# Optimization experiments

Measured on AMD Instinct MI355X. Metric: run time of the kernel, lower is better.

## Reference

```python
import jax, jax.numpy as jnp
import numpy as np

D = 1024
H = 16
DH = D // H  # 64

def setup_inputs() -> dict:
    key = jax.random.key(0)
    ks = jax.random.split(key, 9)
    B, L = 2, 2048
    s = 1.0 / np.sqrt(D)
    inp = {
        'x':  jax.random.normal(ks[0], (B, L, D), dtype=jnp.float32),
        'Wq': jax.random.uniform(ks[1], (D, D), jnp.float32, -s, s),
        'bq': jnp.zeros((D,), jnp.float32),
        'Wk': jax.random.uniform(ks[2], (D, D), jnp.float32, -s, s),
        'bk': jnp.zeros((D,), jnp.float32),
        'Wv': jax.random.uniform(ks[3], (D, D), jnp.float32, -s, s),
        'bv': jnp.zeros((D,), jnp.float32),
        'Wo': jax.random.uniform(ks[4], (D, D), jnp.float32, -s, s),
        'bo': jnp.zeros((D,), jnp.float32),
    }
    return inp

def reference(x, Wq, bq, Wk, bk, Wv, bv, Wo, bo):
    B, L, _ = x.shape
    # projections (torch Linear: x @ W.T + b; here weights stored as [D_in, D_out])
    q = (x @ Wq + bq).reshape(B, L, H, DH).transpose(0, 2, 1, 3)  # [B,H,L,DH]
    k = (x @ Wk + bk).reshape(B, L, H, DH).transpose(0, 2, 1, 3)
    v = (x @ Wv + bv).reshape(B, L, H, DH).transpose(0, 2, 1, 3)
    scores = jnp.einsum('bhqd,bhkd->bhqk', q, k) / jnp.sqrt(jnp.float32(DH))
    attn = jax.nn.softmax(scores, axis=-1)  # dropout p=0 / eval -> identity
    out = jnp.einsum('bhqk,bhkd->bhqd', attn, v)
    out = out.transpose(0, 2, 1, 3).reshape(B, L, D)
    return out @ Wo + bo
```

## Files before the change

### kernel.cpp

```cpp
#include <hip/hip_runtime.h>
#include <stdint.h>

typedef __attribute__((ext_vector_type(8)))  __bf16 bf16x8;
typedef __attribute__((ext_vector_type(4)))  __bf16 bf16x4;
typedef __attribute__((ext_vector_type(4)))  float  f32x4;
typedef __attribute__((ext_vector_type(16))) float  f32x16;
typedef __attribute__((ext_vector_type(4)))  int    i32x4;

#define DEV static __device__ __forceinline__

DEV float fast_exp2(float x) {
#if __has_builtin(__builtin_amdgcn_exp2f)
  return __builtin_amdgcn_exp2f(x);
#else
  return exp2f(x);
#endif
}

DEV uint32_t pack_bf2(float a, float b) {
  __bf16 x = (__bf16)a, y = (__bf16)b;
  uint16_t xu = __builtin_bit_cast(uint16_t, x);
  uint16_t yu = __builtin_bit_cast(uint16_t, y);
  return (uint32_t)xu | ((uint32_t)yu << 16);
}

DEV void gload_lds16(const void* g, void* l) {
  __builtin_amdgcn_global_load_lds(
      (const __attribute__((address_space(1))) void*)(uintptr_t)(g),
      (__attribute__((address_space(3))) void*)(uint32_t)(uintptr_t)(l),
      16, 0, 0);
}

__global__ void k_cvt_x(const float* __restrict__ x, __bf16* __restrict__ xb, int n) {
  int i = (blockIdx.x * 256 + threadIdx.x) * 4;
  if (i < n) {
    f32x4 v = *(const f32x4*)(x + i);
    bf16x4 o;
    o[0] = (__bf16)v[0]; o[1] = (__bf16)v[1];
    o[2] = (__bf16)v[2]; o[3] = (__bf16)v[3];
    *(bf16x4*)(xb + i) = o;
  }
}

__global__ void k_cvt_wt(const float* __restrict__ W, __bf16* __restrict__ Wt,
                         int K, int N) {
  __shared__ __bf16 T[64][66];
  int t = threadIdx.x;
  int r = t >> 2;
  int cq = (t & 3) << 4;
  {
    int gk = blockIdx.y * 64 + r;
    int gn0 = blockIdx.x * 64 + cq;
    const float* src = W + (size_t)gk * N + gn0;
#pragma unroll
    for (int j = 0; j < 16; j += 4) {
      f32x4 v = *(const f32x4*)(src + j);
#pragma unroll
      for (int jj = 0; jj < 4; ++jj) T[r][cq + j + jj] = (__bf16)v[jj];
    }
  }
  __syncthreads();
  {
    int gn = blockIdx.x * 64 + r;
    int gk0 = blockIdx.y * 64 + cq;
    __bf16* dst = Wt + (size_t)gn * K + gk0;
    bf16x8 o0, o1;
#pragma unroll
    for (int j = 0; j < 8; ++j) { o0[j] = T[cq + j][r]; o1[j] = T[cq + 8 + j][r]; }
    *(bf16x8*)dst = o0;
    *(bf16x8*)(dst + 8) = o1;
  }
}

__global__ void k_vt(const __bf16* __restrict__ qkv, __bf16* __restrict__ Vt) {
  __shared__ __bf16 T[64][66];
  int lt = blockIdx.x, bh = blockIdx.y;
  int b = bh >> 4, h = bh & 15;
  int t = threadIdx.x;
  int r = t >> 2, cq = (t & 3) << 4;
  {
    const __bf16* src = qkv + (size_t)(b * 2048 + lt * 64 + r) * 3072 + 2048 + h * 64 + cq;
    bf16x8 v0 = *(const bf16x8*)src;
    bf16x8 v1 = *(const bf16x8*)(src + 8);
#pragma unroll
    for (int j = 0; j < 8; ++j) { T[r][cq + j] = v0[j]; T[r][cq + 8 + j] = v1[j]; }
  }
  __syncthreads();
  {
    __bf16* dst = Vt + (size_t)(bh * 64 + r) * 2048 + lt * 64 + cq;
    bf16x8 o0, o1;
#pragma unroll
    for (int j = 0; j < 8; ++j) { o0[j] = T[cq + j][r]; o1[j] = T[cq + 8 + j][r]; }
    *(bf16x8*)dst = o0;
    *(bf16x8*)(dst + 8) = o1;
  }
}

template <int OUTMODE>
__global__ void k_gemm(const __bf16* __restrict__ A, const __bf16* __restrict__ Bt,
                       void* __restrict__ Cout, int M, int N, int K,
                       const float* __restrict__ b0, const float* __restrict__ b1,
                       const float* __restrict__ b2) {
  __shared__ __align__(16) __bf16 As[128 * 64];
  __shared__ __align__(16) __bf16 Bs[128 * 64];
  const int t = threadIdx.x, wid = t >> 6, lane = t & 63;
  const int bm = blockIdx.y, bn = blockIdx.x;
  const int wm = wid >> 1, wn = wid & 1;
  const int l15 = lane & 15, l4 = lane >> 4;
  const int rr = lane >> 3, cc = lane & 7;
  f32x4 acc[4][4] = {};
  const int nk = K >> 6;
  for (int kt = 0; kt < nk; ++kt) {
    __syncthreads();
#pragma unroll
    for (int j = 0; j < 4; ++j) {
      int row = wid * 32 + j * 8 + rr;
      int csrc = (cc ^ (row & 7)) * 8;
      gload_lds16(A + (size_t)(bm * 128 + row) * K + kt * 64 + csrc,
                  (char*)As + (wid * 32 + j * 8) * 128);
      gload_lds16(Bt + (size_t)(bn * 128 + row) * K + kt * 64 + csrc,
                  (char*)Bs + (wid * 32 + j * 8) * 128);
    }
    __syncthreads();
#pragma unroll
    for (int kk = 0; kk < 2; ++kk) {
      bf16x8 a[4], b[4];
#pragma unroll
      for (int ms = 0; ms < 4; ++ms) {
        int row = wm * 64 + ms * 16 + l15;
        a[ms] = *(const bf16x8*)((char*)As + row * 128 + (((kk * 4 + l4) ^ (row & 7)) * 16));
      }
#pragma unroll
      for (int ns = 0; ns < 4; ++ns) {
        int row = wn * 64 + ns * 16 + l15;
        b[ns] = *(const bf16x8*)((char*)Bs + row * 128 + (((kk * 4 + l4) ^ (row & 7)) * 16));
      }
#pragma unroll
      for (int ms = 0; ms < 4; ++ms)
#pragma unroll
        for (int ns = 0; ns < 4; ++ns)
          acc[ms][ns] = __builtin_amdgcn_mfma_f32_16x16x32_bf16(a[ms], b[ns], acc[ms][ns], 0, 0, 0);
    }
  }
#pragma unroll
  for (int ms = 0; ms < 4; ++ms) {
#pragma unroll
    for (int ns = 0; ns < 4; ++ns) {
      int n = bn * 128 + wn * 64 + ns * 16 + l15;
      float bias;
      if (OUTMODE == 0) {
        const float* bp = (n < 1024) ? b0 : ((n < 2048) ? b1 : b2);
        bias = bp[n & 1023];
      } else {
        bias = b0[n];
      }
#pragma unroll
      for (int i = 0; i < 4; ++i) {
        int m = bm * 128 + wm * 64 + ms * 16 + l4 * 4 + i;
        float v = acc[ms][ns][i] + bias;
        if (OUTMODE == 0) ((__bf16*)Cout)[(size_t)m * N + n] = (__bf16)v;
        else              ((float*)Cout)[(size_t)m * N + n] = v;
      }
    }
  }
}

__global__ void __launch_bounds__(512, 2)
k_attn(const __bf16* __restrict__ qkv, const __bf16* __restrict__ Vt,
       __bf16* __restrict__ Aout) {
  __shared__ __align__(16) char smem[65536];
  const int t = threadIdx.x, w = t >> 6, lane = t & 63;
  const int wq = w & 3, half = w >> 2;
  const int l31 = lane & 31, hi = lane >> 5;
  const int rr = lane >> 3, cc = lane & 7;
  const int qt = blockIdx.x, bh = blockIdx.y;
  const int b = bh >> 4, h = bh & 15;
  const int kv0 = half * 1024;

  const __bf16* Kg = qkv + (size_t)(b * 2048) * 3072 + 1024 + h * 64;
  const __bf16* Vg = Vt + (size_t)(bh * 64) * 2048;

  bf16x8 aq[4];
  {
    int qrow = b * 2048 + qt * 128 + wq * 32 + l31;
    const __bf16* qp = qkv + (size_t)qrow * 3072 + h * 64 + hi * 8;
#pragma unroll
    for (int d = 0; d < 4; ++d) aq[d] = *(const bf16x8*)(qp + d * 16);
  }

  f32x16 o[2] = {};
  float ls[16];
#pragma unroll
  for (int r = 0; r < 16; ++r) ls[r] = 0.f;
  const float C = 0.18033688f;

  auto STAGE = [&](int bi, int kt) {
    char* Kl = smem + half * 32768 + bi * 16384;
    char* Vl = Kl + 8192;
    const __bf16* kg = Kg + (size_t)(kv0 + kt * 64) * 3072;
    const __bf16* vg = Vg + kv0 + kt * 64;
#pragma unroll
    for (int jj = 0; jj < 2; ++jj) {
      int row = wq * 16 + jj * 8 + rr;
      int csrc = (cc ^ (row & 7)) * 8;
      gload_lds16(kg + (size_t)row * 3072 + csrc, Kl + (wq * 16 + jj * 8) * 128);
      gload_lds16(vg + (size_t)row * 2048 + csrc, Vl + (wq * 16 + jj * 8) * 128);
    }
  };

  STAGE(0, 0);
  __syncthreads();

  int cur = 0;
  for (int kt = 0; kt < 16; ++kt) {
    if (kt < 15) STAGE(cur ^ 1, kt + 1);
    char* Kl = smem + half * 32768 + cur * 16384;
    char* Vl = Kl + 8192;

    f32x16 s[2];
    s[0] = 0.f; s[1] = 0.f;
#pragma unroll
    for (int ks = 0; ks < 2; ++ks) {
      int krow = ks * 32 + l31;
#pragma unroll
      for (int d = 0; d < 4; ++d) {
        bf16x8 kf = *(const bf16x8*)(Kl + krow * 128 + (((d * 2 + hi) ^ (krow & 7)) * 16));
        s[ks] = __builtin_amdgcn_mfma_f32_32x32x16_bf16(kf, aq[d], s[ks], 0, 0, 0);
      }
    }

#pragma unroll
    for (int ks = 0; ks < 2; ++ks)
#pragma unroll
      for (int r = 0; r < 16; ++r)
        s[ks][r] = fast_exp2(s[ks][r] * C);

#pragma unroll
    for (int r = 0; r < 16; ++r) ls[r] += s[0][r] + s[1][r];

    uint32_t W[2][8];
#pragma unroll
    for (int ks = 0; ks < 2; ++ks)
#pragma unroll
      for (int c = 0; c < 8; ++c)
        W[ks][c] = pack_bf2(s[ks][2 * c], s[ks][2 * c + 1]);

#pragma unroll
    for (int kstep = 0; kstep < 4; ++kstep) {
      const int ks = kstep >> 1, base = 4 * (kstep & 1);
      uint32_t w0 = W[ks][base + 0], w1 = W[ks][base + 1];
      uint32_t w2 = W[ks][base + 2], w3 = W[ks][base + 3];
      uint32_t x0 = __shfl_xor((int)w0, 32);
      uint32_t x1 = __shfl_xor((int)w1, 32);
      uint32_t x2 = __shfl_xor((int)w2, 32);
      uint32_t x3 = __shfl_xor((int)w3, 32);
      i32x4 pw;
      pw[0] = (int)(hi ? x2 : w0);
      pw[1] = (int)(hi ? x3 : w1);
      pw[2] = (int)(hi ? w2 : x0);
      pw[3] = (int)(hi ? w3 : x1);
      bf16x8 pa = __builtin_bit_cast(bf16x8, pw);
#pragma unroll
      for (int db = 0; db < 2; ++db) {
        int vrow = db * 32 + l31;
        bf16x8 vf = *(const bf16x8*)(Vl + vrow * 128 + (((kstep * 2 + hi) ^ (vrow & 7)) * 16));
        o[db] = __builtin_amdgcn_mfma_f32_32x32x16_bf16(pa, vf, o[db], 0, 0, 0);
      }
    }

    __syncthreads();
    cur ^= 1;
  }

#pragma unroll
  for (int st = 8; st > 0; st >>= 1)
#pragma unroll
    for (int r = 0; r < st; ++r) ls[r] += ls[r + st];
  float rowsum = ls[0] + __shfl_xor(ls[0], 32);

  float* oLDS = (float*)smem;
  float* sLDS = (float*)(smem + 32768);
  sLDS[w * 64 + lane] = rowsum;
  if (w >= 4) {
    float* ob = oLDS + (w - 4) * 2048;
#pragma unroll
    for (int db = 0; db < 2; ++db)
#pragma unroll
      for (int r = 0; r < 16; ++r)
        ob[(db * 16 + r) * 64 + lane] = o[db][r];
  }
  __syncthreads();
  if (w < 4) {
#pragma unroll
    for (int r = 0; r < 16; ++r) {
      int rowq = (r & 3) + 8 * (r >> 2) + 4 * hi;
      float rs1 = __shfl(rowsum, rowq);
      float rs2 = sLDS[(w + 4) * 64 + rowq];
      float inv = 1.0f / (rs1 + rs2);
      int qg = b * 2048 + qt * 128 + wq * 32 + rowq;
#pragma unroll
      for (int db = 0; db < 2; ++db) {
        float o2 = oLDS[w * 2048 + (db * 16 + r) * 64 + lane];
        float v = (o[db][r] + o2) * inv;
        int col = h * 64 + db * 32 + l31;
        Aout[(size_t)qg * 1024 + col] = (__bf16)v;
      }
    }
  }
}

extern "C" void kernel_launch(void* const* d_in, const int* in_sizes, int n_in,
                              void* d_out, int out_size, void* d_ws, size_t ws_size,
                              hipStream_t stream) {
  const float* x  = (const float*)d_in[0];
  const float* Wq = (const float*)d_in[1];
  const float* bq = (const float*)d_in[2];
  const float* Wk = (const float*)d_in[3];
  const float* bk = (const float*)d_in[4];
  const float* Wv = (const float*)d_in[5];
  const float* bv = (const float*)d_in[6];
  const float* Wo = (const float*)d_in[7];
  const float* bo = (const float*)d_in[8];
  float* out = (float*)d_out;

  char* ws = (char*)d_ws;
  __bf16* xb   = (__bf16*)(ws);
  __bf16* wtq  = (__bf16*)(ws + (8ull  << 20));
  __bf16* wot  = (__bf16*)(ws + (14ull << 20));
  __bf16* qkv  = (__bf16*)(ws + (16ull << 20));
  __bf16* vt   = (__bf16*)(ws + (40ull << 20));
  __bf16* aout = (__bf16*)(ws + (48ull << 20));

  k_cvt_x<<<4096, 256, 0, stream>>>(x, xb, 4096 * 1024);

  dim3 wgrid(16, 16);
  k_cvt_wt<<<wgrid, 256, 0, stream>>>(Wq, wtq,               1024, 1024);
  k_cvt_wt<<<wgrid, 256, 0, stream>>>(Wk, wtq + 1024 * 1024, 1024, 1024);
  k_cvt_wt<<<wgrid, 256, 0, stream>>>(Wv, wtq + 2048 * 1024, 1024, 1024);
  k_cvt_wt<<<wgrid, 256, 0, stream>>>(Wo, wot,               1024, 1024);

  k_gemm<0><<<dim3(24, 32), 256, 0, stream>>>(xb, wtq, qkv, 4096, 3072, 1024, bq, bk, bv);

  k_vt<<<dim3(32, 32), 256, 0, stream>>>(qkv, vt);

  k_attn<<<dim3(16, 32), 512, 0, stream>>>(qkv, vt, aout);

  k_gemm<1><<<dim3(8, 32), 256, 0, stream>>>(aout, wot, out, 4096, 1024, 1024, bo, nullptr, nullptr);
}
```

Measured before the change: 132.5 us.

## Fuse prep kernels, remap attention blocks, reorder K/V LDS layout, add MFMA priority

Merges the x-conversion and four weight-transpose kernels into a single k_prep launch that uses a 3D grid, cutting five launches down to one. The attention grid becomes 1D with a remapped block index so that consecutive blocks share query tiles across 8 heads, which may change L2 locality. The K/V staging now stores tiles in LDS in an MFMA-fragment order instead of the XOR-swizzled row layout, so each lane's fragment read is a contiguous lane*16 offset. It also wraps the MFMA sections in s_setprio to favour matrix issue. The new LDS layout has to match the operand layout exactly, which is a correctness risk.

```diff
diff --git a/kernel.cpp b/kernel.cpp
--- a/kernel.cpp
+++ b/kernel.cpp
@@ -31,44 +31,50 @@
       16, 0, 0);
 }
 
-__global__ void k_cvt_x(const float* __restrict__ x, __bf16* __restrict__ xb, int n) {
-  int i = (blockIdx.x * 256 + threadIdx.x) * 4;
-  if (i < n) {
-    f32x4 v = *(const f32x4*)(x + i);
-    bf16x4 o;
-    o[0] = (__bf16)v[0]; o[1] = (__bf16)v[1];
-    o[2] = (__bf16)v[2]; o[3] = (__bf16)v[3];
-    *(bf16x4*)(xb + i) = o;
-  }
-}
-
-__global__ void k_cvt_wt(const float* __restrict__ W, __bf16* __restrict__ Wt,
-                         int K, int N) {
-  __shared__ __bf16 T[64][66];
-  int t = threadIdx.x;
-  int r = t >> 2;
-  int cq = (t & 3) << 4;
-  {
-    int gk = blockIdx.y * 64 + r;
-    int gn0 = blockIdx.x * 64 + cq;
-    const float* src = W + (size_t)gk * N + gn0;
-#pragma unroll
-    for (int j = 0; j < 16; j += 4) {
-      f32x4 v = *(const f32x4*)(src + j);
-#pragma unroll
-      for (int jj = 0; jj < 4; ++jj) T[r][cq + j + jj] = (__bf16)v[jj];
-    }
-  }
-  __syncthreads();
-  {
-    int gn = blockIdx.x * 64 + r;
-    int gk0 = blockIdx.y * 64 + cq;
-    __bf16* dst = Wt + (size_t)gn * K + gk0;
-    bf16x8 o0, o1;
-#pragma unroll
-    for (int j = 0; j < 8; ++j) { o0[j] = T[cq + j][r]; o1[j] = T[cq + 8 + j][r]; }
-    *(bf16x8*)dst = o0;
-    *(bf16x8*)(dst + 8) = o1;
+__global__ void k_prep(const float* __restrict__ x,  __bf16* __restrict__ xb,
+                       const float* __restrict__ Wq, const float* __restrict__ Wk,
+                       const float* __restrict__ Wv, const float* __restrict__ Wo,
+                       __bf16* __restrict__ wtq, __bf16* __restrict__ wot) {
+  const int z = blockIdx.z;
+  if (z < 4) {
+    const float* W  = (z == 0) ? Wq : (z == 1) ? Wk : (z == 2) ? Wv : Wo;
+    __bf16*      Wt = (z == 3) ? wot : (wtq + (size_t)z * 1024 * 1024);
+    __shared__ __bf16 T[64][66];
+    int t = threadIdx.x;
+    int r = t >> 2;
+    int cq = (t & 3) << 4;
+    {
+      int gk = blockIdx.y * 64 + r;
+      int gn0 = blockIdx.x * 64 + cq;
+      const float* src = W + (size_t)gk * 1024 + gn0;
+#pragma unroll
+      for (int j = 0; j < 16; j += 4) {
+        f32x4 v = *(const f32x4*)(src + j);
+#pragma unroll
+        for (int jj = 0; jj < 4; ++jj) T[r][cq + j + jj] = (__bf16)v[jj];
+      }
+    }
+    __syncthreads();
+    {
+      int gn = blockIdx.x * 64 + r;
+      int gk0 = blockIdx.y * 64 + cq;
+      __bf16* dst = Wt + (size_t)gn * 1024 + gk0;
+      bf16x8 o0, o1;
+#pragma unroll
+      for (int j = 0; j < 8; ++j) { o0[j] = T[cq + j][r]; o1[j] = T[cq + 8 + j][r]; }
+      *(bf16x8*)dst = o0;
+      *(bf16x8*)(dst + 8) = o1;
+    }
+  } else {
+    int lb = (z - 4) * 256 + blockIdx.y * 16 + blockIdx.x;
+    int i = (lb * 256 + (int)threadIdx.x) * 4;
+    if (i < 4096 * 1024) {
+      f32x4 v = *(const f32x4*)(x + i);
+      bf16x4 o;
+      o[0] = (__bf16)v[0]; o[1] = (__bf16)v[1];
+      o[2] = (__bf16)v[2]; o[3] = (__bf16)v[3];
+      *(bf16x4*)(xb + i) = o;
+    }
   }
 }
 
@@ -172,8 +178,9 @@
   const int t = threadIdx.x, w = t >> 6, lane = t & 63;
   const int wq = w & 3, half = w >> 2;
   const int l31 = lane & 31, hi = lane >> 5;
-  const int rr = lane >> 3, cc = lane & 7;
-  const int qt = blockIdx.x, bh = blockIdx.y;
+  const int f = blockIdx.x;
+  const int qt = (f >> 3) & 15;
+  const int bh = (f & 7) + 8 * (f >> 7);
   const int b = bh >> 4, h = bh & 15;
   const int kv0 = half * 1024;
 
@@ -198,13 +205,14 @@
     char* Kl = smem + half * 32768 + bi * 16384;
     char* Vl = Kl + 8192;
     const __bf16* kg = Kg + (size_t)(kv0 + kt * 64) * 3072;
-    const __bf16* vg = Vg + kv0 + kt * 64;
+    const __bf16* vg = Vg + (kv0 + kt * 64);
 #pragma unroll
     for (int jj = 0; jj < 2; ++jj) {
-      int row = wq * 16 + jj * 8 + rr;
-      int csrc = (cc ^ (row & 7)) * 8;
-      gload_lds16(kg + (size_t)row * 3072 + csrc, Kl + (wq * 16 + jj * 8) * 128);
-      gload_lds16(vg + (size_t)row * 2048 + csrc, Vl + (wq * 16 + jj * 8) * 128);
+      int idx = (wq * 2 + jj) * 64 + lane;
+      int row = (idx >> 8) * 32 + (idx & 31);
+      int col = ((idx >> 5) & 7) * 8;
+      gload_lds16(kg + (size_t)row * 3072 + col, Kl + (wq * 2 + jj) * 1024);
+      gload_lds16(vg + (size_t)row * 2048 + col, Vl + (wq * 2 + jj) * 1024);
     }
   };
 
@@ -216,18 +224,20 @@
     if (kt < 15) STAGE(cur ^ 1, kt + 1);
     char* Kl = smem + half * 32768 + cur * 16384;
     char* Vl = Kl + 8192;
+    const char* Kv = Kl + lane * 16;
+    const char* Vv = Vl + lane * 16;
 
     f32x16 s[2];
     s[0] = 0.f; s[1] = 0.f;
-#pragma unroll
-    for (int ks = 0; ks < 2; ++ks) {
-      int krow = ks * 32 + l31;
+    __builtin_amdgcn_s_setprio(1);
+#pragma unroll
+    for (int ks = 0; ks < 2; ++ks)
 #pragma unroll
       for (int d = 0; d < 4; ++d) {
-        bf16x8 kf = *(const bf16x8*)(Kl + krow * 128 + (((d * 2 + hi) ^ (krow & 7)) * 16));
+        bf16x8 kf = *(const bf16x8*)(Kv + ks * 4096 + d * 1024);
         s[ks] = __builtin_amdgcn_mfma_f32_32x32x16_bf16(kf, aq[d], s[ks], 0, 0, 0);
       }
-    }
+    __builtin_amdgcn_s_setprio(0);
 
 #pragma unroll
     for (int ks = 0; ks < 2; ++ks)
@@ -260,12 +270,13 @@
       pw[2] = (int)(hi ? w2 : x0);
       pw[3] = (int)(hi ? w3 : x1);
       bf16x8 pa = __builtin_bit_cast(bf16x8, pw);
+      __builtin_amdgcn_s_setprio(1);
 #pragma unroll
       for (int db = 0; db < 2; ++db) {
-        int vrow = db * 32 + l31;
-        bf16x8 vf = *(const bf16x8*)(Vl + vrow * 128 + (((kstep * 2 + hi) ^ (vrow & 7)) * 16));
+        bf16x8 vf = *(const bf16x8*)(Vv + db * 4096 + kstep * 1024);
         o[db] = __builtin_amdgcn_mfma_f32_32x32x16_bf16(pa, vf, o[db], 0, 0, 0);
       }
+      __builtin_amdgcn_s_setprio(0);
     }
 
     __syncthreads();
@@ -331,19 +342,13 @@
   __bf16* vt   = (__bf16*)(ws + (40ull << 20));
   __bf16* aout = (__bf16*)(ws + (48ull << 20));
 
-  k_cvt_x<<<4096, 256, 0, stream>>>(x, xb, 4096 * 1024);
-
-  dim3 wgrid(16, 16);
-  k_cvt_wt<<<wgrid, 256, 0, stream>>>(Wq, wtq,               1024, 1024);
-  k_cvt_wt<<<wgrid, 256, 0, stream>>>(Wk, wtq + 1024 * 1024, 1024, 1024);
-  k_cvt_wt<<<wgrid, 256, 0, stream>>>(Wv, wtq + 2048 * 1024, 1024, 1024);
-  k_cvt_wt<<<wgrid, 256, 0, stream>>>(Wo, wot,               1024, 1024);
+  k_prep<<<dim3(16, 16, 20), 256, 0, stream>>>(x, xb, Wq, Wk, Wv, Wo, wtq, wot);
 
   k_gemm<0><<<dim3(24, 32), 256, 0, stream>>>(xb, wtq, qkv, 4096, 3072, 1024, bq, bk, bv);
 
   k_vt<<<dim3(32, 32), 256, 0, stream>>>(qkv, vt);
 
-  k_attn<<<dim3(16, 32), 512, 0, stream>>>(qkv, vt, aout);
+  k_attn<<<dim3(512), 512, 0, stream>>>(qkv, vt, aout);
 
   k_gemm<1><<<dim3(8, 32), 256, 0, stream>>>(aout, wot, out, 4096, 1024, 1024, bo, nullptr, nullptr);
 }
```

New measurement: 118.8 us. 10.4% less time.
